# Kernel optimization log

Hardware: AMD Instinct MI355X
Metric: run time of the kernel (lower is better)

## Reference

```python
import jax, jax.numpy as jnp
import numpy as np

B, T, I, H, D = 256, 256, 64, 512, 256  # batch, seq_len, input_size, lstm_units, dense_units
R_ON = 0.05    # time-gate open ratio
ALPHA = 1e-3   # leak during closed phase
LN_EPS = 1e-5


def setup_inputs() -> dict:
    key = jax.random.key(0)
    ks = jax.random.split(key, 12)
    sc_in = 1.0 / np.sqrt(I)
    sc_h = 1.0 / np.sqrt(H)
    return {
        "x":  jax.random.normal(ks[0], (B, T, I), dtype=jnp.float32),
        # PLSTM weights (4 gates: i, f, g, o)
        "W":  jax.random.uniform(ks[1], (I, 4 * H), minval=-sc_in, maxval=sc_in, dtype=jnp.float32),
        "U":  jax.random.uniform(ks[2], (H, 4 * H), minval=-sc_h, maxval=sc_h, dtype=jnp.float32),
        "b":  jnp.zeros((4 * H,), dtype=jnp.float32),
        # Phased-LSTM time-gate parameters (per hidden unit)
        "tau": jnp.exp(jax.random.uniform(ks[3], (H,), minval=0.0, maxval=3.0, dtype=jnp.float32)),
        "s":   jax.random.uniform(ks[4], (H,), minval=0.0, maxval=10.0, dtype=jnp.float32),
        # LayerNorm
        "ln_gamma": jnp.ones((H,), dtype=jnp.float32),
        "ln_beta":  jnp.zeros((H,), dtype=jnp.float32),
        # Dense head
        "W1": jax.random.uniform(ks[5], (H, D), minval=-sc_h, maxval=sc_h, dtype=jnp.float32),
        "b1": jnp.zeros((D,), dtype=jnp.float32),
        "W2": jax.random.uniform(ks[6], (D, 1), minval=-1.0 / np.sqrt(D), maxval=1.0 / np.sqrt(D), dtype=jnp.float32),
        "b2": jnp.zeros((1,), dtype=jnp.float32),
    }


def _plstm_last_h(x, W, U, b, tau, s):
    # x: [B, T, I] -> last hidden state [B, H] of the phased LSTM
    xT = jnp.swapaxes(x, 0, 1)                 # [T, B, I]
    times = jnp.arange(x.shape[1], dtype=x.dtype)  # timestamps 0..T-1

    def step(carry, inp):
        h, c = carry
        x_t, t = inp
        z = x_t @ W + h @ U + b                # [B, 4H]
        i_g, f_g, g_g, o_g = jnp.split(z, 4, axis=-1)
        c_tilde = jax.nn.sigmoid(f_g) * c + jax.nn.sigmoid(i_g) * jnp.tanh(g_g)
        h_tilde = jax.nn.sigmoid(o_g) * jnp.tanh(c_tilde)
        # time gate k(t): piecewise-linear oscillation, per hidden unit
        phi = jnp.mod(t - s, tau) / tau        # [H]
        k = jnp.where(phi < 0.5 * R_ON, 2.0 * phi / R_ON,
             jnp.where(phi < R_ON, 2.0 - 2.0 * phi / R_ON, ALPHA * phi))
        c_new = k * c_tilde + (1.0 - k) * c
        h_new = k * h_tilde + (1.0 - k) * h
        return (h_new, c_new), None

    h0 = jnp.zeros((x.shape[0], tau.shape[0]), dtype=x.dtype)
    (h_last, _), _ = jax.lax.scan(step, (h0, h0), (xT, times))
    return h_last


def reference(x, W, U, b, tau, s, ln_gamma, ln_beta, W1, b1, W2, b2):
    h = _plstm_last_h(x, W, U, b, tau, s)      # [B, H] (== out[:, -1, :])
    # LayerNorm over hidden dim (per-position, so applying to last step is exact)
    mu = jnp.mean(h, axis=-1, keepdims=True)
    var = jnp.var(h, axis=-1, keepdims=True)
    hn = (h - mu) * jax.lax.rsqrt(var + LN_EPS) * ln_gamma + ln_beta
    # dropout layers are identity in eval mode
    out = hn @ W1 + b1
    out = out @ W2 + b2                        # [B, 1]
    return out
```

## Files before the change

kernel.cpp:

```cpp
#include <hip/hip_runtime.h>
#include <cmath>

#define NB 256
#define NT 512
#define NG 16
#define GB 16
#define B_ 256
#define T_ 256
#define I_ 64
#define H_ 512
#define G4H 2048
#define BT 16
#define UT 32
#define ZP 132
#define NFC 18
#define CPQ 17
#define CSTR 68
#define NCELL 1224
#define R_ON_F 0.05f
#define ALPHA_F 1.0e-3f
#define LN_EPS_F 1.0e-5f

typedef _Float16 h8 __attribute__((ext_vector_type(8)));
typedef _Float16 h4v __attribute__((ext_vector_type(4)));
typedef float f4 __attribute__((ext_vector_type(4)));
typedef unsigned u4 __attribute__((ext_vector_type(4)));
typedef unsigned short us4 __attribute__((ext_vector_type(4)));

__device__ __align__(16) unsigned g_hp[2][B_ * H_];
__device__ __align__(16) float g_hf[B_ * H_];

struct alignas(256) PadCnt { unsigned v; unsigned pad[63]; };
__device__ PadCnt g_flag[NG][GB];
__device__ unsigned g_launch_cnt;

__device__ __forceinline__ float fast_sigmoid(float x) {
    return __builtin_amdgcn_rcpf(1.f + __expf(-x));
}
__device__ __forceinline__ float fast_tanh(float x) {
    return 1.f - 2.f * __builtin_amdgcn_rcpf(__expf(2.f * x) + 1.f);
}

struct HiLo { _Float16 hi, lo; };
__device__ __forceinline__ HiLo cvt_hilo(float v) {
    HiLo r;
    r.hi = (_Float16)v;
    r.lo = (_Float16)(v - (float)r.hi);
    return r;
}

__global__ __launch_bounds__(NT, 1) void plstm_scan_kernel(
    const float* __restrict__ x, const float* __restrict__ W,
    const float* __restrict__ U, const float* __restrict__ bias,
    const float* __restrict__ tau, const float* __restrict__ sph,
    const float* __restrict__ ln_g, const float* __restrict__ ln_b,
    const float* __restrict__ W1, const float* __restrict__ b1,
    const float* __restrict__ W2, const float* __restrict__ b2,
    float* __restrict__ out)
{
    __shared__ __align__(16) _Float16 Ah[NCELL * 8];
    __shared__ __align__(16) float zs[BT][ZP];
    __shared__ __align__(16) float kt[T_ * UT];
    __shared__ float red[16];
    __shared__ unsigned s_tag;

    const int tid = threadIdx.x;
    const int bt = blockIdx.x >> 4;
    const int ut = blockIdx.x & 15;
    const int b0 = bt * BT;
    const int u0 = ut * UT;

    if (tid == 0) s_tag = (atomicAdd(&g_launch_cnt, 1u) >> 8) + 1u;

    const int wv = tid >> 6;
    const int lane = tid & 63;
    const int n_ = lane & 15;
    const int q_ = lane >> 4;

    const int jg = (wv >> 1) * 512 + u0 + (wv & 1) * 16 + n_;
    h8 Bh[NFC], Bl[NFC];
    #pragma unroll
    for (int c = 0; c < NFC; ++c) {
        #pragma unroll
        for (int e = 0; e < 8; ++e) {
            const int kk = c * 32 + q_ * 8 + e;
            float v;
            if (c < 2) v = W[(size_t)kk * G4H + jg];
            else       v = U[(size_t)(kk - I_) * G4H + jg];
            const HiLo hl = cvt_hilo(v);
            Bh[c][e] = hl.hi;
            Bl[c][e] = hl.lo;
        }
    }
    const float bv = bias[jg];

    for (int idx = tid; idx < T_ * UT; idx += NT) {
        const int tt = idx >> 5, ul = idx & 31;
        const float ta = tau[u0 + ul];
        float aa = (float)tt - sph[u0 + ul];
        float rr = fmodf(aa, ta);
        if (rr < 0.f) rr += ta;
        const float phi = rr / ta;
        float kk;
        if (phi < 0.5f * R_ON_F)      kk = phi * (2.f / R_ON_F);
        else if (phi < R_ON_F)        kk = 2.f - phi * (2.f / R_ON_F);
        else                          kk = ALPHA_F * phi;
        kt[idx] = kk;
    }
    __syncthreads();
    const unsigned tagw = s_tag;
    const unsigned tagb = (tagw & 0xFFu) << 8;

    const int urow = tid >> 5;
    const int uu   = tid & 31;
    float c_st = 0.f;
    float h_st = 0.f;

    const int xr = (tid >> 4) & 15, xc4 = (tid & 15) << 2;
    const int cX = (tid & 15) >> 3, qX = ((tid & 15) >> 1) & 3;
    const int e0x = (tid & 1) << 2;
    const int fX = (cX * CSTR + qX * CPQ + xr) * 8 + e0x;
    const int m = tid & 127;
    const int hr0 = tid >> 7;
    const int hk4 = m << 2;
    const int cS = 2 + (m >> 3), qS = (m >> 1) & 3;
    const int e0 = (m & 1) << 2;

    float4 xv = *(const float4*)(x + ((size_t)(b0 + xr) * T_ + 0) * I_ + xc4);

    const int fb = (q_ * CPQ + n_) * 8;

    int cur = 0;
    for (int t = 0; t < T_; ++t) {
        if (t == 0) {
            const h8 z8 = {};
            for (int idx = tid; idx < NCELL; idx += NT)
                *(h8*)&Ah[idx * 8] = z8;
            __syncthreads();
            if (tid < 256) {
                h4v xh;
                xh[0] = (_Float16)xv.x; xh[1] = (_Float16)xv.y;
                xh[2] = (_Float16)xv.z; xh[3] = (_Float16)xv.w;
                *(h4v*)&Ah[fX] = xh;
            }
        } else {
            const unsigned* hb = g_hp[cur] + (size_t)(b0 + hr0) * H_ + hk4;
            const unsigned want = tagb | (unsigned)t;
            u4 a0, a1, a2, a3;
            bool ok;
            do {
                asm volatile(
                    "global_load_dwordx4 %0, %4, off sc0 sc1\n\t"
                    "global_load_dwordx4 %1, %5, off sc0 sc1\n\t"
                    "global_load_dwordx4 %2, %6, off sc0 sc1\n\t"
                    "global_load_dwordx4 %3, %7, off sc0 sc1\n\t"
                    "s_waitcnt vmcnt(0)"
                    : "=&v"(a0), "=&v"(a1), "=&v"(a2), "=&v"(a3)
                    : "v"(hb), "v"(hb + 4 * H_), "v"(hb + 8 * H_), "v"(hb + 12 * H_)
                    : "memory");
                ok = ((a0[0] & 0xFFFFu) == want) & ((a0[1] & 0xFFFFu) == want)
                   & ((a0[2] & 0xFFFFu) == want) & ((a0[3] & 0xFFFFu) == want)
                   & ((a1[0] & 0xFFFFu) == want) & ((a1[1] & 0xFFFFu) == want)
                   & ((a1[2] & 0xFFFFu) == want) & ((a1[3] & 0xFFFFu) == want)
                   & ((a2[0] & 0xFFFFu) == want) & ((a2[1] & 0xFFFFu) == want)
                   & ((a2[2] & 0xFFFFu) == want) & ((a2[3] & 0xFFFFu) == want)
                   & ((a3[0] & 0xFFFFu) == want) & ((a3[1] & 0xFFFFu) == want)
                   & ((a3[2] & 0xFFFFu) == want) & ((a3[3] & 0xFFFFu) == want);
            } while (__ballot(!ok));
            const u4 av[4] = {a0, a1, a2, a3};
            #pragma unroll
            for (int it = 0; it < 4; ++it) {
                const int row = hr0 + 4 * it;
                const int fidx = (cS * CSTR + qS * CPQ + row) * 8 + e0;
                us4 uv;
                uv[0] = (unsigned short)(av[it][0] >> 16);
                uv[1] = (unsigned short)(av[it][1] >> 16);
                uv[2] = (unsigned short)(av[it][2] >> 16);
                uv[3] = (unsigned short)(av[it][3] >> 16);
                *(us4*)&Ah[fidx] = uv;
            }
        }
        __syncthreads();

        if (tid < 256) {
            const int tn = (t < T_ - 1) ? t + 1 : t;
            xv = *(const float4*)(x + ((size_t)(b0 + xr) * T_ + tn) * I_ + xc4);
        }

        f4 ac0 = {bv, bv, bv, bv};
        f4 ac1 = {0.f, 0.f, 0.f, 0.f};
        #pragma unroll
        for (int c = 0; c < NFC; ++c) {
            const h8 ah = *(const h8*)&Ah[fb + c * (CSTR * 8)];
            ac0 = __builtin_amdgcn_mfma_f32_16x16x32_f16(ah, Bh[c], ac0, 0, 0, 0);
            ac1 = __builtin_amdgcn_mfma_f32_16x16x32_f16(ah, Bl[c], ac1, 0, 0, 0);
        }
        const f4 zt = ac0 + ac1;
        {
            const int colz = wv * 16 + n_;
            const int rz = q_ * 4;
            zs[rz + 0][colz] = zt[0];
            zs[rz + 1][colz] = zt[1];
            zs[rz + 2][colz] = zt[2];
            zs[rz + 3][colz] = zt[3];
        }
        __syncthreads();

        {
            const float zi = zs[urow][uu];
            const float zf = zs[urow][32 + uu];
            const float zg = zs[urow][64 + uu];
            const float zo = zs[urow][96 + uu];
            const float si = fast_sigmoid(zi);
            const float sf = fast_sigmoid(zf);
            const float so = fast_sigmoid(zo);
            const float ct = sf * c_st + si * fast_tanh(zg);
            const float ht = so * fast_tanh(ct);
            const float kk = kt[(t << 5) + uu];
            const float hn = kk * ht + (1.f - kk) * h_st;
            c_st = kk * ct + (1.f - kk) * c_st;
            h_st = hn;
            if (t < T_ - 1) {
                const unsigned short hb16 = __builtin_bit_cast(unsigned short, (_Float16)hn);
                const unsigned packed = ((unsigned)hb16 << 16) | (tagb | (unsigned)(t + 1));
                unsigned* gp = g_hp[cur ^ 1] + (size_t)(b0 + urow) * H_ + (u0 + uu);
                asm volatile("global_store_dword %0, %1, off sc0 sc1"
                             :: "v"(gp), "v"(packed) : "memory");
            } else {
                float* gp = g_hf + (size_t)(b0 + urow) * H_ + (u0 + uu);
                asm volatile("global_store_dword %0, %1, off sc0 sc1\n\ts_waitcnt vmcnt(0)"
                             :: "v"(gp), "v"(hn) : "memory");
            }
        }

        if (t == T_ - 1) {
            __syncthreads();
            if (tid == 0) {
                unsigned fv = (tagw << 8) | 0xFFu;
                asm volatile("global_store_dword %0, %1, off sc0 sc1"
                             :: "v"(&g_flag[bt][ut].v), "v"(fv) : "memory");
            }
        }

        if (t < T_ - 1 && tid < 256) {
            h4v xh;
            xh[0] = (_Float16)xv.x; xh[1] = (_Float16)xv.y;
            xh[2] = (_Float16)xv.z; xh[3] = (_Float16)xv.w;
            *(h4v*)&Ah[fX] = xh;
        }
        cur ^= 1;
    }

    {
        if (tid < 64) {
            const unsigned want = (tagw << 8) | 0xFFu;
            const unsigned* fp = &g_flag[bt][tid & 15].v;
            unsigned v;
            do {
                asm volatile("global_load_dword %0, %1, off sc0 sc1\n\ts_waitcnt vmcnt(0)"
                             : "=v"(v) : "v"(fp) : "memory");
            } while (__ballot(v != want));
        }
        __syncthreads();

        const int r = b0 + ut;
        float hv;
        const float* hp = g_hf + (size_t)r * H_ + tid;
        asm volatile("global_load_dword %0, %1, off sc0 sc1\n\ts_waitcnt vmcnt(0)"
                     : "=v"(hv) : "v"(hp) : "memory");
        float s1 = hv, s2 = hv * hv;
        #pragma unroll
        for (int off = 32; off > 0; off >>= 1) {
            s1 += __shfl_down(s1, off, 64);
            s2 += __shfl_down(s2, off, 64);
        }
        const int ln = tid & 63;
        if (ln == 0) { red[wv] = s1; red[8 + wv] = s2; }
        __syncthreads();
        float S1 = 0.f, S2 = 0.f;
        #pragma unroll
        for (int w = 0; w < 8; ++w) { S1 += red[w]; S2 += red[8 + w]; }
        const float mu = S1 * (1.f / 512.f);
        const float var = S2 * (1.f / 512.f) - mu * mu;
        const float rstd = rsqrtf(var + LN_EPS_F);
        const float hn = (hv - mu) * rstd * ln_g[tid] + ln_b[tid];
        float w12 = 0.f;
        const float* w1p = W1 + (size_t)tid * 256;
        #pragma unroll 4
        for (int d = 0; d < 256; ++d) w12 = fmaf(w1p[d], W2[d], w12);
        float contrib = hn * w12;
        if (tid < 256) contrib = fmaf(b1[tid], W2[tid], contrib);
        #pragma unroll
        for (int off = 32; off > 0; off >>= 1) contrib += __shfl_down(contrib, off, 64);
        __syncthreads();
        if (ln == 0) red[wv] = contrib;
        __syncthreads();
        if (tid == 0) {
            float tot = b2[0];
            #pragma unroll
            for (int w = 0; w < 8; ++w) tot += red[w];
            out[r] = tot;
        }
    }
}

extern "C" void kernel_launch(void* const* d_in, const int* in_sizes, int n_in,
                              void* d_out, int out_size, void* d_ws, size_t ws_size,
                              hipStream_t stream) {
    const float* x   = (const float*)d_in[0];
    const float* W   = (const float*)d_in[1];
    const float* U   = (const float*)d_in[2];
    const float* b   = (const float*)d_in[3];
    const float* tau = (const float*)d_in[4];
    const float* s   = (const float*)d_in[5];
    const float* lng = (const float*)d_in[6];
    const float* lnb = (const float*)d_in[7];
    const float* W1  = (const float*)d_in[8];
    const float* b1  = (const float*)d_in[9];
    const float* W2  = (const float*)d_in[10];
    const float* b2  = (const float*)d_in[11];
    float* out = (float*)d_out;
    plstm_scan_kernel<<<dim3(NB), dim3(NT), 0, stream>>>(
        x, W, U, b, tau, s, lng, lnb, W1, b1, W2, b2, out);
}
```

Baseline: 764.2 us.

## Interleave two batch tiles per block to hide cross-block recurrence latency

Halves the grid to 128 blocks, and each block now processes two batch tiles (p and p+8) in alternation within every timestep. While one tile waits for its peers' hidden state through global-memory polling, the other tile computes, so the inter-block synchronization latency is meant to overlap with useful MFMA work. This doubles the serial per-block work per step and adds extra barriers. It also depends on at most 128 co-resident blocks for the spin-wait protocol, and the launch tag derivation is changed to match.

```diff
diff --git a/kernel.cpp b/kernel.cpp
--- a/kernel.cpp
+++ b/kernel.cpp
@@ -1,10 +1,11 @@
 #include <hip/hip_runtime.h>
 #include <cmath>
 
-#define NB 256
+#define NB 128
 #define NT 512
 #define NG 16
 #define GB 16
+#define NPAIR 8
 #define B_ 256
 #define T_ 256
 #define I_ 64
@@ -49,6 +50,45 @@
     return r;
 }
 
+__device__ __forceinline__ void poll_stage(const unsigned* hb, unsigned want,
+                                           _Float16* AhB, int hr0,
+                                           int cS, int qS, int e0)
+{
+    u4 a0, a1, a2, a3;
+    bool ok;
+    do {
+        asm volatile(
+            "global_load_dwordx4 %0, %4, off sc0 sc1\n\t"
+            "global_load_dwordx4 %1, %5, off sc0 sc1\n\t"
+            "global_load_dwordx4 %2, %6, off sc0 sc1\n\t"
+            "global_load_dwordx4 %3, %7, off sc0 sc1\n\t"
+            "s_waitcnt vmcnt(0)"
+            : "=&v"(a0), "=&v"(a1), "=&v"(a2), "=&v"(a3)
+            : "v"(hb), "v"(hb + 4 * H_), "v"(hb + 8 * H_), "v"(hb + 12 * H_)
+            : "memory");
+        ok = ((a0[0] & 0xFFFFu) == want) & ((a0[1] & 0xFFFFu) == want)
+           & ((a0[2] & 0xFFFFu) == want) & ((a0[3] & 0xFFFFu) == want)
+           & ((a1[0] & 0xFFFFu) == want) & ((a1[1] & 0xFFFFu) == want)
+           & ((a1[2] & 0xFFFFu) == want) & ((a1[3] & 0xFFFFu) == want)
+           & ((a2[0] & 0xFFFFu) == want) & ((a2[1] & 0xFFFFu) == want)
+           & ((a2[2] & 0xFFFFu) == want) & ((a2[3] & 0xFFFFu) == want)
+           & ((a3[0] & 0xFFFFu) == want) & ((a3[1] & 0xFFFFu) == want)
+           & ((a3[2] & 0xFFFFu) == want) & ((a3[3] & 0xFFFFu) == want);
+    } while (__ballot(!ok));
+    const u4 av[4] = {a0, a1, a2, a3};
+    #pragma unroll
+    for (int it = 0; it < 4; ++it) {
+        const int row = hr0 + 4 * it;
+        const int fidx = (cS * CSTR + qS * CPQ + row) * 8 + e0;
+        us4 uv;
+        uv[0] = (unsigned short)(av[it][0] >> 16);
+        uv[1] = (unsigned short)(av[it][1] >> 16);
+        uv[2] = (unsigned short)(av[it][2] >> 16);
+        uv[3] = (unsigned short)(av[it][3] >> 16);
+        *(us4*)&AhB[fidx] = uv;
+    }
+}
+
 __global__ __launch_bounds__(NT, 1) void plstm_scan_kernel(
     const float* __restrict__ x, const float* __restrict__ W,
     const float* __restrict__ U, const float* __restrict__ bias,
@@ -65,12 +105,13 @@
     __shared__ unsigned s_tag;
 
     const int tid = threadIdx.x;
-    const int bt = blockIdx.x >> 4;
+    const int p  = blockIdx.x >> 4;
     const int ut = blockIdx.x & 15;
-    const int b0 = bt * BT;
+    const int b0A = p * BT;
+    const int b0B = (p + NPAIR) * BT;
     const int u0 = ut * UT;
 
-    if (tid == 0) s_tag = (atomicAdd(&g_launch_cnt, 1u) >> 8) + 1u;
+    if (tid == 0) s_tag = (atomicAdd(&g_launch_cnt, 1u) >> 7) + 1u;
 
     const int wv = tid >> 6;
     const int lane = tid & 63;
@@ -107,14 +148,11 @@
         else                          kk = ALPHA_F * phi;
         kt[idx] = kk;
     }
-    __syncthreads();
-    const unsigned tagw = s_tag;
-    const unsigned tagb = (tagw & 0xFFu) << 8;
 
     const int urow = tid >> 5;
     const int uu   = tid & 31;
-    float c_st = 0.f;
-    float h_st = 0.f;
+    float cA = 0.f, hA = 0.f;
+    float cB = 0.f, hB = 0.f;
 
     const int xr = (tid >> 4) & 15, xc4 = (tid & 15) << 2;
     const int cX = (tid & 15) >> 3, qX = ((tid & 15) >> 1) & 3;
@@ -126,77 +164,47 @@
     const int cS = 2 + (m >> 3), qS = (m >> 1) & 3;
     const int e0 = (m & 1) << 2;
 
-    float4 xv = *(const float4*)(x + ((size_t)(b0 + xr) * T_ + 0) * I_ + xc4);
+    {
+        const h8 z8 = {};
+        for (int idx = tid; idx < NCELL; idx += NT)
+            *(h8*)&Ah[idx * 8] = z8;
+    }
+    float4 xvA = {}, xvB = {};
+    if (tid < 256) {
+        xvA = *(const float4*)(x + ((size_t)(b0A + xr) * T_ + 0) * I_ + xc4);
+        xvB = *(const float4*)(x + ((size_t)(b0B + xr) * T_ + 0) * I_ + xc4);
+    }
+    __syncthreads();
+    const unsigned tagw = s_tag;
+    const unsigned tagb = (tagw & 0xFFu) << 8;
+    if (tid < 256) {
+        h4v xh;
+        xh[0] = (_Float16)xvA.x; xh[1] = (_Float16)xvA.y;
+        xh[2] = (_Float16)xvA.z; xh[3] = (_Float16)xvA.w;
+        *(h4v*)&Ah[fX] = xh;
+    }
 
     const int fb = (q_ * CPQ + n_) * 8;
 
     int cur = 0;
     for (int t = 0; t < T_; ++t) {
-        if (t == 0) {
-            const h8 z8 = {};
-            for (int idx = tid; idx < NCELL; idx += NT)
-                *(h8*)&Ah[idx * 8] = z8;
-            __syncthreads();
-            if (tid < 256) {
-                h4v xh;
-                xh[0] = (_Float16)xv.x; xh[1] = (_Float16)xv.y;
-                xh[2] = (_Float16)xv.z; xh[3] = (_Float16)xv.w;
-                *(h4v*)&Ah[fX] = xh;
-            }
-        } else {
-            const unsigned* hb = g_hp[cur] + (size_t)(b0 + hr0) * H_ + hk4;
-            const unsigned want = tagb | (unsigned)t;
-            u4 a0, a1, a2, a3;
-            bool ok;
-            do {
-                asm volatile(
-                    "global_load_dwordx4 %0, %4, off sc0 sc1\n\t"
-                    "global_load_dwordx4 %1, %5, off sc0 sc1\n\t"
-                    "global_load_dwordx4 %2, %6, off sc0 sc1\n\t"
-                    "global_load_dwordx4 %3, %7, off sc0 sc1\n\t"
-                    "s_waitcnt vmcnt(0)"
-                    : "=&v"(a0), "=&v"(a1), "=&v"(a2), "=&v"(a3)
-                    : "v"(hb), "v"(hb + 4 * H_), "v"(hb + 8 * H_), "v"(hb + 12 * H_)
-                    : "memory");
-                ok = ((a0[0] & 0xFFFFu) == want) & ((a0[1] & 0xFFFFu) == want)
-                   & ((a0[2] & 0xFFFFu) == want) & ((a0[3] & 0xFFFFu) == want)
-                   & ((a1[0] & 0xFFFFu) == want) & ((a1[1] & 0xFFFFu) == want)
-                   & ((a1[2] & 0xFFFFu) == want) & ((a1[3] & 0xFFFFu) == want)
-                   & ((a2[0] & 0xFFFFu) == want) & ((a2[1] & 0xFFFFu) == want)
-                   & ((a2[2] & 0xFFFFu) == want) & ((a2[3] & 0xFFFFu) == want)
-                   & ((a3[0] & 0xFFFFu) == want) & ((a3[1] & 0xFFFFu) == want)
-                   & ((a3[2] & 0xFFFFu) == want) & ((a3[3] & 0xFFFFu) == want);
-            } while (__ballot(!ok));
-            const u4 av[4] = {a0, a1, a2, a3};
-            #pragma unroll
-            for (int it = 0; it < 4; ++it) {
-                const int row = hr0 + 4 * it;
-                const int fidx = (cS * CSTR + qS * CPQ + row) * 8 + e0;
-                us4 uv;
-                uv[0] = (unsigned short)(av[it][0] >> 16);
-                uv[1] = (unsigned short)(av[it][1] >> 16);
-                uv[2] = (unsigned short)(av[it][2] >> 16);
-                uv[3] = (unsigned short)(av[it][3] >> 16);
-                *(us4*)&Ah[fidx] = uv;
-            }
-        }
-        __syncthreads();
-
-        if (tid < 256) {
-            const int tn = (t < T_ - 1) ? t + 1 : t;
-            xv = *(const float4*)(x + ((size_t)(b0 + xr) * T_ + tn) * I_ + xc4);
-        }
-
-        f4 ac0 = {bv, bv, bv, bv};
-        f4 ac1 = {0.f, 0.f, 0.f, 0.f};
-        #pragma unroll
-        for (int c = 0; c < NFC; ++c) {
-            const h8 ah = *(const h8*)&Ah[fb + c * (CSTR * 8)];
-            ac0 = __builtin_amdgcn_mfma_f32_16x16x32_f16(ah, Bh[c], ac0, 0, 0, 0);
-            ac1 = __builtin_amdgcn_mfma_f32_16x16x32_f16(ah, Bl[c], ac1, 0, 0, 0);
-        }
-        const f4 zt = ac0 + ac1;
+        if (t > 0)
+            poll_stage(g_hp[cur] + (size_t)(b0A + hr0) * H_ + hk4,
+                       tagb | (unsigned)t, Ah, hr0, cS, qS, e0);
+        __syncthreads();
+        if (tid < 256 && t < T_ - 1)
+            xvA = *(const float4*)(x + ((size_t)(b0A + xr) * T_ + t + 1) * I_ + xc4);
+
         {
+            f4 ac0 = {bv, bv, bv, bv};
+            f4 ac1 = {0.f, 0.f, 0.f, 0.f};
+            #pragma unroll
+            for (int c = 0; c < NFC; ++c) {
+                const h8 ah = *(const h8*)&Ah[fb + c * (CSTR * 8)];
+                ac0 = __builtin_amdgcn_mfma_f32_16x16x32_f16(ah, Bh[c], ac0, 0, 0, 0);
+                ac1 = __builtin_amdgcn_mfma_f32_16x16x32_f16(ah, Bl[c], ac1, 0, 0, 0);
+            }
+            const f4 zt = ac0 + ac1;
             const int colz = wv * 16 + n_;
             const int rz = q_ * 4;
             zs[rz + 0][colz] = zt[0];
@@ -206,6 +214,7 @@
         }
         __syncthreads();
 
+        const float kk = kt[(t << 5) + uu];
         {
             const float zi = zs[urow][uu];
             const float zf = zs[urow][32 + uu];
@@ -214,47 +223,104 @@
             const float si = fast_sigmoid(zi);
             const float sf = fast_sigmoid(zf);
             const float so = fast_sigmoid(zo);
-            const float ct = sf * c_st + si * fast_tanh(zg);
+            const float ct = sf * cA + si * fast_tanh(zg);
             const float ht = so * fast_tanh(ct);
-            const float kk = kt[(t << 5) + uu];
-            const float hn = kk * ht + (1.f - kk) * h_st;
-            c_st = kk * ct + (1.f - kk) * c_st;
-            h_st = hn;
+            const float hn = kk * ht + (1.f - kk) * hA;
+            cA = kk * ct + (1.f - kk) * cA;
+            hA = hn;
             if (t < T_ - 1) {
                 const unsigned short hb16 = __builtin_bit_cast(unsigned short, (_Float16)hn);
                 const unsigned packed = ((unsigned)hb16 << 16) | (tagb | (unsigned)(t + 1));
-                unsigned* gp = g_hp[cur ^ 1] + (size_t)(b0 + urow) * H_ + (u0 + uu);
+                unsigned* gp = g_hp[cur ^ 1] + (size_t)(b0A + urow) * H_ + (u0 + uu);
                 asm volatile("global_store_dword %0, %1, off sc0 sc1"
                              :: "v"(gp), "v"(packed) : "memory");
             } else {
-                float* gp = g_hf + (size_t)(b0 + urow) * H_ + (u0 + uu);
+                float* gp = g_hf + (size_t)(b0A + urow) * H_ + (u0 + uu);
                 asm volatile("global_store_dword %0, %1, off sc0 sc1\n\ts_waitcnt vmcnt(0)"
                              :: "v"(gp), "v"(hn) : "memory");
             }
         }
-
-        if (t == T_ - 1) {
-            __syncthreads();
-            if (tid == 0) {
-                unsigned fv = (tagw << 8) | 0xFFu;
+        if (t > 0)
+            poll_stage(g_hp[cur] + (size_t)(b0B + hr0) * H_ + hk4,
+                       tagb | (unsigned)t, Ah, hr0, cS, qS, e0);
+        if (tid < 256) {
+            h4v xh;
+            xh[0] = (_Float16)xvB.x; xh[1] = (_Float16)xvB.y;
+            xh[2] = (_Float16)xvB.z; xh[3] = (_Float16)xvB.w;
+            *(h4v*)&Ah[fX] = xh;
+        }
+        __syncthreads();
+        if (tid < 256 && t < T_ - 1)
+            xvB = *(const float4*)(x + ((size_t)(b0B + xr) * T_ + t + 1) * I_ + xc4);
+
+        {
+            f4 ac0 = {bv, bv, bv, bv};
+            f4 ac1 = {0.f, 0.f, 0.f, 0.f};
+            #pragma unroll
+            for (int c = 0; c < NFC; ++c) {
+                const h8 ah = *(const h8*)&Ah[fb + c * (CSTR * 8)];
+                ac0 = __builtin_amdgcn_mfma_f32_16x16x32_f16(ah, Bh[c], ac0, 0, 0, 0);
+                ac1 = __builtin_amdgcn_mfma_f32_16x16x32_f16(ah, Bl[c], ac1, 0, 0, 0);
+            }
+            const f4 zt = ac0 + ac1;
+            const int colz = wv * 16 + n_;
+            const int rz = q_ * 4;
+            zs[rz + 0][colz] = zt[0];
+            zs[rz + 1][colz] = zt[1];
+            zs[rz + 2][colz] = zt[2];
+            zs[rz + 3][colz] = zt[3];
+        }
+        __syncthreads();
+
+        {
+            const float zi = zs[urow][uu];
+            const float zf = zs[urow][32 + uu];
+            const float zg = zs[urow][64 + uu];
+            const float zo = zs[urow][96 + uu];
+            const float si = fast_sigmoid(zi);
+            const float sf = fast_sigmoid(zf);
+            const float so = fast_sigmoid(zo);
+            const float ct = sf * cB + si * fast_tanh(zg);
+            const float ht = so * fast_tanh(ct);
+            const float hn = kk * ht + (1.f - kk) * hB;
+            cB = kk * ct + (1.f - kk) * cB;
+            hB = hn;
+            if (t < T_ - 1) {
+                const unsigned short hb16 = __builtin_bit_cast(unsigned short, (_Float16)hn);
+                const unsigned packed = ((unsigned)hb16 << 16) | (tagb | (unsigned)(t + 1));
+                unsigned* gp = g_hp[cur ^ 1] + (size_t)(b0B + urow) * H_ + (u0 + uu);
                 asm volatile("global_store_dword %0, %1, off sc0 sc1"
-                             :: "v"(&g_flag[bt][ut].v), "v"(fv) : "memory");
-            }
-        }
-
-        if (t < T_ - 1 && tid < 256) {
+                             :: "v"(gp), "v"(packed) : "memory");
+            } else {
+                float* gp = g_hf + (size_t)(b0B + urow) * H_ + (u0 + uu);
+                asm volatile("global_store_dword %0, %1, off sc0 sc1\n\ts_waitcnt vmcnt(0)"
+                             :: "v"(gp), "v"(hn) : "memory");
+            }
+        }
+        if (tid < 256 && t < T_ - 1) {
             h4v xh;
-            xh[0] = (_Float16)xv.x; xh[1] = (_Float16)xv.y;
-            xh[2] = (_Float16)xv.z; xh[3] = (_Float16)xv.w;
+            xh[0] = (_Float16)xvA.x; xh[1] = (_Float16)xvA.y;
+            xh[2] = (_Float16)xvA.z; xh[3] = (_Float16)xvA.w;
             *(h4v*)&Ah[fX] = xh;
         }
         cur ^= 1;
+    }
+
+    __syncthreads();
+    if (tid == 0) {
+        const unsigned fv = (tagw << 8) | 0xFFu;
+        asm volatile("global_store_dword %0, %2, off sc0 sc1\n\t"
+                     "global_store_dword %1, %2, off sc0 sc1"
+                     :: "v"(&g_flag[p][ut].v), "v"(&g_flag[p + NPAIR][ut].v), "v"(fv)
+                     : "memory");
     }
 
     {
         if (tid < 64) {
             const unsigned want = (tagw << 8) | 0xFFu;
-            const unsigned* fp = &g_flag[bt][tid & 15].v;
+            const int idx = tid & 31;
+            const unsigned* fp = (idx < 16) ? &g_flag[p][idx].v
+                                            : &g_flag[p + NPAIR][idx - 16].v;
             unsigned v;
             do {
                 asm volatile("global_load_dword %0, %1, off sc0 sc1\n\ts_waitcnt vmcnt(0)"
@@ -263,43 +329,48 @@
         }
         __syncthreads();
 
-        const int r = b0 + ut;
-        float hv;
-        const float* hp = g_hf + (size_t)r * H_ + tid;
-        asm volatile("global_load_dword %0, %1, off sc0 sc1\n\ts_waitcnt vmcnt(0)"
-                     : "=v"(hv) : "v"(hp) : "memory");
-        float s1 = hv, s2 = hv * hv;
-        #pragma unroll
-        for (int off = 32; off > 0; off >>= 1) {
-            s1 += __shfl_down(s1, off, 64);
-            s2 += __shfl_down(s2, off, 64);
-        }
-        const int ln = tid & 63;
-        if (ln == 0) { red[wv] = s1; red[8 + wv] = s2; }
-        __syncthreads();
-        float S1 = 0.f, S2 = 0.f;
-        #pragma unroll
-        for (int w = 0; w < 8; ++w) { S1 += red[w]; S2 += red[8 + w]; }
-        const float mu = S1 * (1.f / 512.f);
-        const float var = S2 * (1.f / 512.f) - mu * mu;
-        const float rstd = rsqrtf(var + LN_EPS_F);
-        const float hn = (hv - mu) * rstd * ln_g[tid] + ln_b[tid];
         float w12 = 0.f;
         const float* w1p = W1 + (size_t)tid * 256;
         #pragma unroll 4
         for (int d = 0; d < 256; ++d) w12 = fmaf(w1p[d], W2[d], w12);
-        float contrib = hn * w12;
-        if (tid < 256) contrib = fmaf(b1[tid], W2[tid], contrib);
-        #pragma unroll
-        for (int off = 32; off > 0; off >>= 1) contrib += __shfl_down(contrib, off, 64);
-        __syncthreads();
-        if (ln == 0) red[wv] = contrib;
-        __syncthreads();
-        if (tid == 0) {
-            float tot = b2[0];
-            #pragma unroll
-            for (int w = 0; w < 8; ++w) tot += red[w];
-            out[r] = tot;
+        const float bterm = (tid < 256) ? b1[tid] * W2[tid] : 0.f;
+        const int ln = tid & 63;
+
+        #pragma unroll 1
+        for (int rep = 0; rep < 2; ++rep) {
+            const int r = (rep ? b0B : b0A) + ut;
+            float hv;
+            const float* hp = g_hf + (size_t)r * H_ + tid;
+            asm volatile("global_load_dword %0, %1, off sc0 sc1\n\ts_waitcnt vmcnt(0)"
+                         : "=v"(hv) : "v"(hp) : "memory");
+            float s1 = hv, s2 = hv * hv;
+            #pragma unroll
+            for (int off = 32; off > 0; off >>= 1) {
+                s1 += __shfl_down(s1, off, 64);
+                s2 += __shfl_down(s2, off, 64);
+            }
+            if (ln == 0) { red[wv] = s1; red[8 + wv] = s2; }
+            __syncthreads();
+            float S1 = 0.f, S2 = 0.f;
+            #pragma unroll
+            for (int w = 0; w < 8; ++w) { S1 += red[w]; S2 += red[8 + w]; }
+            const float mu = S1 * (1.f / 512.f);
+            const float var = S2 * (1.f / 512.f) - mu * mu;
+            const float rstd = rsqrtf(var + LN_EPS_F);
+            const float hn = (hv - mu) * rstd * ln_g[tid] + ln_b[tid];
+            float contrib = hn * w12 + bterm;
+            #pragma unroll
+            for (int off = 32; off > 0; off >>= 1) contrib += __shfl_down(contrib, off, 64);
+            __syncthreads();
+            if (ln == 0) red[wv] = contrib;
+            __syncthreads();
+            if (tid == 0) {
+                float tot = b2[0];
+                #pragma unroll
+                for (int w = 0; w < 8; ++w) tot += red[w];
+                out[r] = tot;
+            }
+            __syncthreads();
         }
     }
 }
```

New measurement: 1.051 ms. 37.6% more time.
